# Kernel tuning notes

Measured on AMD Instinct MI355X. Metric: run time of the kernel, lower is better.

Reference implementation:

```python
import jax, jax.numpy as jnp
import numpy as np

EPS = 1e-6  # T5LayerNorm epsilon


def setup_inputs() -> dict:
    key = jax.random.key(0)
    k0, k1, k2, k3 = jax.random.split(key, 4)
    B, S, D, F, E = 4, 2048, 768, 3072, 8
    hidden_states = jax.random.normal(k0, (B, S, D), jnp.float32)
    router_w = jax.random.normal(k1, (E, D), jnp.float32) * 0.02
    ln_w = jnp.ones((E, D), jnp.float32)
    wi = jax.random.normal(k2, (E, F, D), jnp.float32) * 0.02
    wo = jax.random.normal(k3, (E, D, F), jnp.float32) * 0.02
    return {"hidden_states": hidden_states, "router_w": router_w, "ln_w": ln_w,
            "wi": wi, "wo": wo, "top_k": 2}


def reference(hidden_states, router_w, ln_w, wi, wo, top_k):
    B, S, D = hidden_states.shape
    E = router_w.shape[0]
    x = hidden_states.reshape(-1, D)                      # [T, D] tokens
    router_logits = x @ router_w.T                        # [T, E]
    probs = jax.nn.softmax(router_logits, axis=-1)
    rw, sel = jax.lax.top_k(probs, top_k)                 # [T, K]
    rw = rw / jnp.sum(rw, axis=-1, keepdims=True)         # renormalize top-k weights

    # T5LayerNorm is RMS-norm (no mean subtraction); shared input x, per-expert scale.
    var = jnp.mean(x * x, axis=-1, keepdims=True)         # [T, 1]
    x_norm = x * jax.lax.rsqrt(var + EPS)                 # [T, D]

    out = jnp.zeros_like(x)
    for e in range(E):  # fixed small loop over experts (structurally distinct params)
        # combine weight for expert e: zero for tokens that did not select it
        w_e = jnp.sum(jnp.where(sel == e, rw, 0.0), axis=-1)   # [T]
        h = x_norm * ln_w[e]                                   # [T, D]
        ff = jax.nn.relu(h @ wi[e].T) @ wo[e].T                # [T, D]
        # T5LayerFF returns x + FFN(LN(x)); routing weight scales the whole output
        out = out + w_e[:, None] * (x + ff)
    layer_output = out.reshape(B, S, D)
    return layer_output, router_logits
```

## Files before the change

kernel.cpp:

```cpp
#include <hip/hip_runtime.h>
#include <hip/hip_bf16.h>
#include <math.h>

typedef short short8 __attribute__((ext_vector_type(8)));
typedef float f32x16 __attribute__((ext_vector_type(16)));

constexpr int D = 768;
constexpr int E = 8;
constexpr int F = 3072;
constexpr int T = 8192;
constexpr float EPS = 1e-6f;

static __device__ inline unsigned short f2bf(float f) {
    __hip_bfloat16 h = __float2bfloat16(f);
    return *reinterpret_cast<unsigned short*>(&h);
}

static __device__ inline f32x16 mfma_bf16(short8 a, short8 b, f32x16 c) {
    return __builtin_amdgcn_mfma_f32_32x32x16_bf16(a, b, c, 0, 0, 0);
}

#define GLL16(g, s) __builtin_amdgcn_global_load_lds( \
    (const __attribute__((address_space(1))) unsigned int*)(g), \
    (__attribute__((address_space(3))) unsigned int*)(s), 16, 0, 0)

__global__ __launch_bounds__(256)
void prep_kernel(const float* __restrict__ wi, const float* __restrict__ wo,
                 const float* __restrict__ lnw,
                 unsigned short* __restrict__ wip, unsigned short* __restrict__ wop,
                 const float* __restrict__ x, const float* __restrict__ rw,
                 float* __restrict__ logits, unsigned short* __restrict__ xn,
                 int* __restrict__ sel, float2* __restrict__ w01)
{
    if (blockIdx.x < 36864) {
        const unsigned NWI = (unsigned)E * F * D;
        unsigned i4 = (blockIdx.x * 256u + threadIdx.x) * 4u;
        if (i4 < NWI) {
            float4 v = *(const float4*)(wi + i4);
            unsigned e = i4 / (unsigned)(F * D);
            unsigned d = i4 % (unsigned)D;
            float4 l = *(const float4*)(lnw + e * D + d);
            ushort4 o = { f2bf(v.x * l.x), f2bf(v.y * l.y), f2bf(v.z * l.z), f2bf(v.w * l.w) };
            *(ushort4*)(wip + i4) = o;
        } else {
            unsigned j = i4 - NWI;
            float4 v = *(const float4*)(wo + j);
            ushort4 o = { f2bf(v.x), f2bf(v.y), f2bf(v.z), f2bf(v.w) };
            *(ushort4*)(wop + j) = o;
        }
        return;
    }

    const int lane = threadIdx.x & 63;
    const int wid  = threadIdx.x >> 6;
    const int t = (blockIdx.x - 36864) * 4 + wid;
    if (t >= T) return;

    const float* xr = x + (size_t)t * D;
    float xv[12];
    float acc[8];
#pragma unroll
    for (int e = 0; e < 8; ++e) acc[e] = 0.f;
    float ssq = 0.f;
#pragma unroll
    for (int i = 0; i < 12; ++i) {
        const int k = lane + 64 * i;
        const float v = xr[k];
        xv[i] = v;
        ssq += v * v;
#pragma unroll
        for (int e = 0; e < 8; ++e) acc[e] += v * rw[e * D + k];
    }
#pragma unroll
    for (int off = 32; off; off >>= 1) {
        ssq += __shfl_xor(ssq, off);
#pragma unroll
        for (int e = 0; e < 8; ++e) acc[e] += __shfl_xor(acc[e], off);
    }

    int e0 = 0; float m0 = acc[0];
#pragma unroll
    for (int e = 1; e < 8; ++e) if (acc[e] > m0) { m0 = acc[e]; e0 = e; }
    int e1 = -1; float m1 = -3.4e38f;
#pragma unroll
    for (int e = 0; e < 8; ++e) if (e != e0 && acc[e] > m1) { m1 = acc[e]; e1 = e; }

    const float r  = expf(m1 - m0);
    const float w0 = 1.f / (1.f + r);
    const float w1 = r * w0;
    const float rs = rsqrtf(ssq * (1.f / (float)D) + EPS);

    if (lane == 0) {
#pragma unroll
        for (int e = 0; e < 8; ++e) logits[t * 8 + e] = acc[e];
        sel[t] = e0 | (e1 << 4);
        w01[t] = make_float2(w0, w1);
    }

#pragma unroll
    for (int i = 0; i < 12; ++i) {
        const int k = lane + 64 * i;
        xn[(size_t)t * D + k] = f2bf(xv[i] * rs);
    }
}

__global__ __launch_bounds__(256)
void lists_kernel(const int* __restrict__ sel, const float2* __restrict__ w01,
                  int* __restrict__ offs,
                  int* __restrict__ lists, float* __restrict__ wlist)
{
    const int e = blockIdx.x;
    const int tid = threadIdx.x;
    const int lane = tid & 63;
    const int wv = tid >> 6;

    __shared__ int sc[4][8];
    __shared__ int wtot[4];

    int c[8];
#pragma unroll
    for (int i = 0; i < 8; ++i) c[i] = 0;
    for (int t = tid; t < T; t += 256) {
        const int s = sel[t];
        const int a = s & 15, b = (s >> 4) & 15;
#pragma unroll
        for (int i = 0; i < 8; ++i) c[i] += (a == i) + (b == i);
    }
#pragma unroll
    for (int off = 32; off; off >>= 1)
#pragma unroll
        for (int i = 0; i < 8; ++i) c[i] += __shfl_xor(c[i], off);
    if (lane == 0)
#pragma unroll
        for (int i = 0; i < 8; ++i) sc[wv][i] = c[i];
    __syncthreads();

    int cnt8[8];
#pragma unroll
    for (int i = 0; i < 8; ++i) cnt8[i] = sc[0][i] + sc[1][i] + sc[2][i] + sc[3][i];
    int base = 0;
#pragma unroll
    for (int i = 0; i < 8; ++i) if (i < e) base += cnt8[i];

    if (e == 0 && tid == 0) {
        int a = 0;
#pragma unroll
        for (int i = 0; i < 8; ++i) { offs[i] = a; a += cnt8[i]; }
        offs[8] = a;
    }

    int cnt = 0;
    for (int c0 = 0; c0 < T; c0 += 256) {
        const int t = c0 + tid;
        const int s = sel[t];
        const bool m1 = ((s >> 4) & 15) == e;
        const bool m = ((s & 15) == e) || m1;
        const unsigned long long b = __ballot(m);
        const int pre = __popcll(b & ((1ULL << lane) - 1ULL));
        if (lane == 0) wtot[wv] = __popcll(b);
        __syncthreads();
        int wbase = 0;
#pragma unroll
        for (int i = 0; i < 4; ++i) if (i < wv) wbase += wtot[i];
        if (m) {
            const int pos = base + cnt + wbase + pre;
            lists[pos] = (t << 1) | (m1 ? 1 : 0);
            const float2 w = w01[t];
            wlist[pos] = m1 ? w.y : w.x;
        }
        cnt += wtot[0] + wtot[1] + wtot[2] + wtot[3];
        __syncthreads();
    }
}

__global__ __launch_bounds__(256)
void gemm1_kernel(const unsigned short* __restrict__ xn,
                  const unsigned short* __restrict__ wip,
                  const int* __restrict__ offs,
                  const int* __restrict__ lists,
                  unsigned short* __restrict__ H)
{
    __shared__ unsigned short sA[128 * 64];
    __shared__ unsigned short sB[128 * 64];
    __shared__ int s_tok[128];

    const int bid = blockIdx.x;
    const int e  = bid & 7;
    const int q  = bid >> 3;
    const int mt = q / 24;
    const int nt = q % 24;
    const int offe = offs[e];
    const int cnt = offs[e + 1] - offe;
    const int base = mt * 128;
    if (base >= cnt) return;

    const int tid = threadIdx.x;
    const int w = tid >> 6, l = tid & 63;
    const int lo = l & 31, hi = l >> 5;
    const int wr = w >> 1, wc = w & 1;

    if (tid < 128) {
        const int idx = base + tid;
        s_tok[tid] = (idx < cnt) ? (lists[offe + idx] >> 1) : 0;
    }
    __syncthreads();

    const int r = (w * 4 + 0) * 8 + (l >> 3);
    const int chS = ((l & 7) ^ ((l >> 3) & 7)) * 8;
    const unsigned short* aSrc[4];
    const unsigned short* bSrc[4];
#pragma unroll
    for (int j = 0; j < 4; ++j) {
        const int rj = r + j * 8;
        aSrc[j] = xn + (size_t)s_tok[rj] * D + chS;
        bSrc[j] = wip + ((size_t)e * F + nt * 128 + rj) * D + chS;
    }
    char* sAc = (char*)sA;
    char* sBc = (char*)sB;

    f32x16 acc00, acc01, acc10, acc11;
#pragma unroll
    for (int qq = 0; qq < 16; ++qq) { acc00[qq] = 0.f; acc01[qq] = 0.f; acc10[qq] = 0.f; acc11[qq] = 0.f; }

    const int rx = (lo & 7) << 4;
    const int arow0 = (wr * 64 + lo) * 128;
    const int arow1 = arow0 + 32 * 128;
    const int brow0 = (wc * 64 + lo) * 128;
    const int brow1 = brow0 + 32 * 128;

    for (int kt = 0; kt < 12; ++kt) {
        const int k0 = kt * 64;
#pragma unroll
        for (int j = 0; j < 4; ++j) {
            GLL16(aSrc[j] + k0, sAc + (w * 4 + j) * 1024);
            GLL16(bSrc[j] + k0, sBc + (w * 4 + j) * 1024);
        }
        __syncthreads();
#pragma unroll
        for (int ks = 0; ks < 4; ++ks) {
            const int coff = (hi * 16 + ks * 32) ^ rx;
            short8 a0 = *(const short8*)(sAc + arow0 + coff);
            short8 a1 = *(const short8*)(sAc + arow1 + coff);
            short8 b0 = *(const short8*)(sBc + brow0 + coff);
            short8 b1 = *(const short8*)(sBc + brow1 + coff);
            acc00 = mfma_bf16(a0, b0, acc00);
            acc01 = mfma_bf16(a0, b1, acc01);
            acc10 = mfma_bf16(a1, b0, acc10);
            acc11 = mfma_bf16(a1, b1, acc11);
        }
        __syncthreads();
    }

    const int cbase = nt * 128 + wc * 64 + lo;
#pragma unroll
    for (int rr = 0; rr < 16; ++rr) {
        const int crow = (rr & 3) + 8 * (rr >> 2) + 4 * hi;
        int lrow = wr * 64 + crow;
        if (base + lrow < cnt) {
            unsigned short* hp = H + (size_t)(offe + base + lrow) * F + cbase;
            hp[0]  = f2bf(fmaxf(acc00[rr], 0.f));
            hp[32] = f2bf(fmaxf(acc01[rr], 0.f));
        }
        lrow += 32;
        if (base + lrow < cnt) {
            unsigned short* hp = H + (size_t)(offe + base + lrow) * F + cbase;
            hp[0]  = f2bf(fmaxf(acc10[rr], 0.f));
            hp[32] = f2bf(fmaxf(acc11[rr], 0.f));
        }
    }
}

__global__ __launch_bounds__(512)
void gemm2_kernel(const unsigned short* __restrict__ H,
                  const unsigned short* __restrict__ wop,
                  const int* __restrict__ offs,
                  const int* __restrict__ lists, const float* __restrict__ wlist,
                  float* __restrict__ ffout0, float* __restrict__ ffout1,
                  int kts)
{
    __shared__ unsigned short sT[384 * 64];
    __shared__ int   s_tok[128];
    __shared__ float s_wgt[128];

    const int bid = blockIdx.x;
    const int e  = bid & 7;
    const int q  = bid >> 3;
    const int kh = q / 192;
    const int rm = q % 192;
    const int mt = rm / 3;
    const int nt = rm % 3;
    const int offe = offs[e];
    const int cnt = offs[e + 1] - offe;
    const int base = mt * 128;
    if (base >= cnt) return;

    const int tid = threadIdx.x;
    const int w = tid >> 6, l = tid & 63;
    const int lo = l & 31, hi = l >> 5;
    const int wr = w >> 2;
    const int wcn = w & 3;

    if (tid < 128) {
        const int idx = base + tid;
        const bool v = idx < cnt;
        s_tok[tid] = v ? lists[offe + idx] : 0;
        s_wgt[tid] = v ? wlist[offe + idx] : 0.f;
    }
    __syncthreads();

    const int kof = kh * kts * 64;
    const int srow = tid >> 3;
    const int chS = ((tid & 7) ^ (srow & 7)) * 8;
    const unsigned short* src6[6];
#pragma unroll
    for (int c = 0; c < 6; ++c) {
        const int rrow = srow + c * 64;
        if (rrow < 128) {
            src6[c] = H + (size_t)(offe + base + rrow) * F + kof + chS;
        } else {
            src6[c] = wop + ((size_t)e * D + nt * 256 + (rrow - 128)) * F + kof + chS;
        }
    }
    char* sTc = (char*)sT;
    const int dOff = srow * 128 + (tid & 7) * 16;

    f32x16 acc00, acc01, acc10, acc11;
#pragma unroll
    for (int qq = 0; qq < 16; ++qq) { acc00[qq] = 0.f; acc01[qq] = 0.f; acc10[qq] = 0.f; acc11[qq] = 0.f; }

    const int rx = (lo & 7) << 4;
    const int arow0 = (wr * 64 + lo) * 128;
    const int arow1 = arow0 + 32 * 128;
    const int brow0 = (128 + wcn * 64 + lo) * 128;
    const int brow1 = brow0 + 32 * 128;

    for (int kt = 0; kt < kts; ++kt) {
        const int k0 = kt * 64;
#pragma unroll
        for (int c = 0; c < 6; ++c)
            GLL16(src6[c] + k0, sTc + c * 8192 + dOff);
        __syncthreads();
#pragma unroll
        for (int ks = 0; ks < 4; ++ks) {
            const int coff = (hi * 16 + ks * 32) ^ rx;
            short8 a0 = *(const short8*)(sTc + arow0 + coff);
            short8 a1 = *(const short8*)(sTc + arow1 + coff);
            short8 b0 = *(const short8*)(sTc + brow0 + coff);
            short8 b1 = *(const short8*)(sTc + brow1 + coff);
            acc00 = mfma_bf16(a0, b0, acc00);
            acc01 = mfma_bf16(a0, b1, acc01);
            acc10 = mfma_bf16(a1, b0, acc10);
            acc11 = mfma_bf16(a1, b1, acc11);
        }
        __syncthreads();
    }

    float* fbase = kh ? ffout1 : ffout0;
    const int cbase = nt * 256 + wcn * 64 + lo;
#pragma unroll
    for (int rr = 0; rr < 16; ++rr) {
        const int crow = (rr & 3) + 8 * (rr >> 2) + 4 * hi;
#pragma unroll
        for (int mh = 0; mh < 2; ++mh) {
            const int lrow = wr * 64 + crow + mh * 32;
            if (base + lrow < cnt) {
                const int pk = s_tok[lrow];
                const float wgt = s_wgt[lrow];
                float* dst = fbase + ((size_t)(pk & 1) * T + (pk >> 1)) * D + cbase;
                dst[0]  = wgt * (mh ? acc10[rr] : acc00[rr]);
                dst[32] = wgt * (mh ? acc11[rr] : acc01[rr]);
            }
        }
    }
}

__global__ __launch_bounds__(256)
void combine_kernel(const float* __restrict__ x, const float2* __restrict__ w01,
                    const float* __restrict__ f0, const float* __restrict__ f1,
                    int nkh, float* __restrict__ out)
{
    const long long i4 = ((long long)blockIdx.x * 256 + threadIdx.x) * 4;
    const int t = (int)(i4 / D);
    const float2 wp = w01[t];
    const float ws = wp.x + wp.y;
    float4 xv = *(const float4*)(x + i4);
    float4 a0 = *(const float4*)(f0 + i4);
    float4 a1 = *(const float4*)(f0 + (long long)T * D + i4);
    float4 o = { ws * xv.x + a0.x + a1.x, ws * xv.y + a0.y + a1.y,
                 ws * xv.z + a0.z + a1.z, ws * xv.w + a0.w + a1.w };
    if (nkh == 2) {
        float4 b0 = *(const float4*)(f1 + i4);
        float4 b1 = *(const float4*)(f1 + (long long)T * D + i4);
        o.x += b0.x + b1.x; o.y += b0.y + b1.y;
        o.z += b0.z + b1.z; o.w += b0.w + b1.w;
    }
    *(float4*)(out + i4) = o;
}

extern "C" void kernel_launch(void* const* d_in, const int* in_sizes, int n_in,
                              void* d_out, int out_size, void* d_ws, size_t ws_size,
                              hipStream_t stream) {
    const float* x   = (const float*)d_in[0];
    const float* rw  = (const float*)d_in[1];
    const float* lnw = (const float*)d_in[2];
    const float* wi  = (const float*)d_in[3];
    const float* wo  = (const float*)d_in[4];

    float* out    = (float*)d_out;
    float* logits = (float*)d_out + (size_t)T * D;

    char* ws = (char*)d_ws;
    unsigned short* xn     = (unsigned short*)(ws);
    unsigned short* wip    = (unsigned short*)(ws + 12582912);
    float*          ffout0 = (float*)(ws);
    unsigned short* wop    = (unsigned short*)(ws + 50331648);
    unsigned short* H      = (unsigned short*)(ws + 88080384);
    int*            offs   = (int*)(ws + 190316544);
    int*            sel    = (int*)(ws + 190316672);
    float2*         w01    = (float2*)(ws + 190349440);
    int*            lists  = (int*)(ws + 190414976);
    float*          wlist  = (float*)(ws + 190480512);
    float*          ffout1 = (float*)(ws + 190578688);

    const bool big2 = ws_size >= 240910336ULL;
    const int nkh = big2 ? 2 : 1;
    const int kts = 48 / nkh;

    prep_kernel<<<36864 + T / 4, 256, 0, stream>>>(wi, wo, lnw, wip, wop,
                                                   x, rw, logits, xn,
                                                   sel, w01);

    lists_kernel<<<E, 256, 0, stream>>>(sel, w01, offs, lists, wlist);

    gemm1_kernel<<<64 * 24 * 8, 256, 0, stream>>>(xn, wip, offs, lists, H);
    gemm2_kernel<<<nkh * 64 * 3 * 8, 512, 0, stream>>>(H, wop, offs, lists,
                                                       wlist, ffout0,
                                                       big2 ? ffout1 : ffout0,
                                                       kts);
    combine_kernel<<<T * D / 4 / 256, 256, 0, stream>>>(x, w01, ffout0,
                                                        big2 ? ffout1 : ffout0,
                                                        nkh, out);
}
```

Before: 316.9 us.

## Widen gemm1 tile to 128x256 with 512-thread blocks sharing one A tile

Result: no change. 317.0 us (+0.0%).

```diff
diff --git a/kernel.cpp b/kernel.cpp
--- a/kernel.cpp
+++ b/kernel.cpp
@@ -173,22 +173,21 @@
     }
 }
 
-__global__ __launch_bounds__(256)
+__global__ __launch_bounds__(512)
 void gemm1_kernel(const unsigned short* __restrict__ xn,
                   const unsigned short* __restrict__ wip,
                   const int* __restrict__ offs,
                   const int* __restrict__ lists,
                   unsigned short* __restrict__ H)
 {
-    __shared__ unsigned short sA[128 * 64];
-    __shared__ unsigned short sB[128 * 64];
+    __shared__ unsigned short sT[384 * 64];
     __shared__ int s_tok[128];
 
     const int bid = blockIdx.x;
     const int e  = bid & 7;
     const int q  = bid >> 3;
-    const int mt = q / 24;
-    const int nt = q % 24;
+    const int mt = q / 12;
+    const int nt = q % 12;
     const int offe = offs[e];
     const int cnt = offs[e + 1] - offe;
     const int base = mt * 128;
@@ -197,7 +196,8 @@
     const int tid = threadIdx.x;
     const int w = tid >> 6, l = tid & 63;
     const int lo = l & 31, hi = l >> 5;
-    const int wr = w >> 1, wc = w & 1;
+    const int wr = w >> 2;
+    const int wcn = w & 3;
 
     if (tid < 128) {
         const int idx = base + tid;
@@ -205,18 +205,20 @@
     }
     __syncthreads();
 
-    const int r = (w * 4 + 0) * 8 + (l >> 3);
-    const int chS = ((l & 7) ^ ((l >> 3) & 7)) * 8;
-    const unsigned short* aSrc[4];
-    const unsigned short* bSrc[4];
-#pragma unroll
-    for (int j = 0; j < 4; ++j) {
-        const int rj = r + j * 8;
-        aSrc[j] = xn + (size_t)s_tok[rj] * D + chS;
-        bSrc[j] = wip + ((size_t)e * F + nt * 128 + rj) * D + chS;
-    }
-    char* sAc = (char*)sA;
-    char* sBc = (char*)sB;
+    const int srow = tid >> 3;
+    const int chS = ((tid & 7) ^ (srow & 7)) * 8;
+    const unsigned short* src6[6];
+#pragma unroll
+    for (int c = 0; c < 6; ++c) {
+        const int rrow = srow + c * 64;
+        if (rrow < 128) {
+            src6[c] = xn + (size_t)s_tok[rrow] * D + chS;
+        } else {
+            src6[c] = wip + ((size_t)e * F + nt * 256 + (rrow - 128)) * D + chS;
+        }
+    }
+    char* sTc = (char*)sT;
+    const int dOff = srow * 128 + (tid & 7) * 16;
 
     f32x16 acc00, acc01, acc10, acc11;
 #pragma unroll
@@ -225,24 +227,22 @@
     const int rx = (lo & 7) << 4;
     const int arow0 = (wr * 64 + lo) * 128;
     const int arow1 = arow0 + 32 * 128;
-    const int brow0 = (wc * 64 + lo) * 128;
+    const int brow0 = (128 + wcn * 64 + lo) * 128;
     const int brow1 = brow0 + 32 * 128;
 
     for (int kt = 0; kt < 12; ++kt) {
         const int k0 = kt * 64;
 #pragma unroll
-        for (int j = 0; j < 4; ++j) {
-            GLL16(aSrc[j] + k0, sAc + (w * 4 + j) * 1024);
-            GLL16(bSrc[j] + k0, sBc + (w * 4 + j) * 1024);
-        }
+        for (int c = 0; c < 6; ++c)
+            GLL16(src6[c] + k0, sTc + c * 8192 + dOff);
         __syncthreads();
 #pragma unroll
         for (int ks = 0; ks < 4; ++ks) {
             const int coff = (hi * 16 + ks * 32) ^ rx;
-            short8 a0 = *(const short8*)(sAc + arow0 + coff);
-            short8 a1 = *(const short8*)(sAc + arow1 + coff);
-            short8 b0 = *(const short8*)(sBc + brow0 + coff);
-            short8 b1 = *(const short8*)(sBc + brow1 + coff);
+            short8 a0 = *(const short8*)(sTc + arow0 + coff);
+            short8 a1 = *(const short8*)(sTc + arow1 + coff);
+            short8 b0 = *(const short8*)(sTc + brow0 + coff);
+            short8 b1 = *(const short8*)(sTc + brow1 + coff);
             acc00 = mfma_bf16(a0, b0, acc00);
             acc01 = mfma_bf16(a0, b1, acc01);
             acc10 = mfma_bf16(a1, b0, acc10);
@@ -251,21 +251,18 @@
         __syncthreads();
     }
 
-    const int cbase = nt * 128 + wc * 64 + lo;
+    const int cbase = nt * 256 + wcn * 64 + lo;
 #pragma unroll
     for (int rr = 0; rr < 16; ++rr) {
         const int crow = (rr & 3) + 8 * (rr >> 2) + 4 * hi;
-        int lrow = wr * 64 + crow;
-        if (base + lrow < cnt) {
-            unsigned short* hp = H + (size_t)(offe + base + lrow) * F + cbase;
-            hp[0]  = f2bf(fmaxf(acc00[rr], 0.f));
-            hp[32] = f2bf(fmaxf(acc01[rr], 0.f));
-        }
-        lrow += 32;
-        if (base + lrow < cnt) {
-            unsigned short* hp = H + (size_t)(offe + base + lrow) * F + cbase;
-            hp[0]  = f2bf(fmaxf(acc10[rr], 0.f));
-            hp[32] = f2bf(fmaxf(acc11[rr], 0.f));
+#pragma unroll
+        for (int mh = 0; mh < 2; ++mh) {
+            const int lrow = wr * 64 + crow + mh * 32;
+            if (base + lrow < cnt) {
+                unsigned short* hp = H + (size_t)(offe + base + lrow) * F + cbase;
+                hp[0]  = f2bf(fmaxf((mh ? acc10[rr] : acc00[rr]), 0.f));
+                hp[32] = f2bf(fmaxf((mh ? acc11[rr] : acc01[rr]), 0.f));
+            }
         }
     }
 }
@@ -432,7 +429,7 @@
 
     lists_kernel<<<E, 256, 0, stream>>>(sel, w01, offs, lists, wlist);
 
-    gemm1_kernel<<<64 * 24 * 8, 256, 0, stream>>>(xn, wip, offs, lists, H);
+    gemm1_kernel<<<64 * 12 * 8, 512, 0, stream>>>(xn, wip, offs, lists, H);
     gemm2_kernel<<<nkh * 64 * 3 * 8, 512, 0, stream>>>(H, wop, offs, lists,
                                                        wlist, ffout0,
                                                        big2 ? ffout1 : ffout0,
```
